# Performance work log

Measured on AMD Instinct MI355X. Metric: run time of the kernel, lower is better.

The kernel has to match this reference:

```python
import jax, jax.numpy as jnp
import numpy as np

B, C, H, W = 16, 64, 48, 48
D = C * W  # xLSTM embedding dim (== C*H since H==W)
K = 5          # phi='S' kernel size
G_CONV = C // 8  # conv groups = 8
G_NORM = 16      # GroupNorm groups
EPS = 1e-5


def setup_inputs() -> dict:
    key = jax.random.key(0)
    ks = jax.random.split(key, 10)
    s = 0.02
    return {
        'x': jax.random.normal(ks[0], (B, C, H, W), jnp.float32),
        'W1': (jax.random.normal(ks[1], (D, 4 * D), jnp.float32) * s),
        'R1': (jax.random.normal(ks[2], (D, 4 * D), jnp.float32) * s),
        'b1': jnp.zeros((4 * D,), jnp.float32),
        'W2': (jax.random.normal(ks[3], (D, 4 * D), jnp.float32) * s),
        'R2': (jax.random.normal(ks[4], (D, 4 * D), jnp.float32) * s),
        'b2': jnp.zeros((4 * D,), jnp.float32),
        'conv_w': jax.random.normal(ks[5], (C, C // G_CONV, K), jnp.float32) * (1.0 / np.sqrt((C // G_CONV) * K)),
        'gn_gamma': jnp.ones((C,), jnp.float32),
        'gn_beta': jnp.zeros((C,), jnp.float32),
    }


def xlstm_stack(x, Wm, Rm, bm):
    """sLSTM-style xLSTM block (exp gating + stabilizer). x: [B,T,D] -> [B,T,D]."""
    Bsz, T, Dm = x.shape
    pre = jnp.einsum('btd,de->bte', x, Wm) + bm  # input projection for all steps

    def step(carry, p):
        h, c, n, m = carry
        g = p + h @ Rm                      # [B,4D]
        it, ft, zt, ot = jnp.split(g, 4, axis=-1)
        m_new = jnp.maximum(ft + m, it)     # stabilizer
        i = jnp.exp(it - m_new)
        f = jnp.exp(ft + m - m_new)
        c_new = f * c + i * jnp.tanh(zt)
        n_new = f * n + i
        h_new = jax.nn.sigmoid(ot) * c_new / (n_new + 1e-6)
        return (h_new, c_new, n_new, m_new), h_new

    z = jnp.zeros((Bsz, Dm), x.dtype)
    _, ys = jax.lax.scan(step, (z, z, z, z), jnp.swapaxes(pre, 0, 1))
    return jnp.swapaxes(ys, 0, 1)  # [B,T,D]


def conv1d_grouped(x, w):
    pad = K // 2
    return jax.lax.conv_general_dilated(
        x, w, window_strides=(1,), padding=[(pad, pad)],
        feature_group_count=G_CONV, dimension_numbers=('NCH', 'OIH', 'NCH'))


def group_norm(x, gamma, beta):
    b, c, L = x.shape
    xg = x.reshape(b, G_NORM, -1)
    mu = xg.mean(-1, keepdims=True)
    var = xg.var(-1, keepdims=True)
    xn = ((xg - mu) * jax.lax.rsqrt(var + EPS)).reshape(b, c, L)
    return xn * gamma[None, :, None] + beta[None, :, None]


def ela_forward(x, W1, R1, b1, W2, R2, b2, conv_w, gn_gamma, gn_beta):
    b, c, h, w = x.shape
    # stack cfg2: sequence over h, features c*w
    y2 = xlstm_stack(x.reshape(b, h, c * w), W2, R2, b2).reshape(b, c, w, h)
    # stack cfg1: sequence over w, features c*h
    y1 = xlstm_stack(x.reshape(b, w, c * h), W1, R1, b1).reshape(b, c, w, h)
    x_h = jnp.mean(y2, axis=3).reshape(b, c, h)
    x_w = jnp.mean(y1, axis=2).reshape(b, c, w)
    x_h = jax.nn.sigmoid(group_norm(conv1d_grouped(x_h, conv_w), gn_gamma, gn_beta)).reshape(b, c, h, 1)
    x_w = jax.nn.sigmoid(group_norm(conv1d_grouped(x_w, conv_w), gn_gamma, gn_beta)).reshape(b, c, 1, w)
    return x_h * x_w * x


def reference(x, W1, R1, b1, W2, R2, b2, conv_w, gn_gamma, gn_beta):
    return ela_forward(x, W1, R1, b1, W2, R2, b2, conv_w, gn_gamma, gn_beta)
```

## Files before the change

### kernel.cpp

```cpp
#include <hip/hip_runtime.h>
#include <hip/hip_bf16.h>


typedef float  f32x4 __attribute__((ext_vector_type(4)));
typedef __bf16 v8bf  __attribute__((ext_vector_type(8)));
typedef __bf16 v4bf  __attribute__((ext_vector_type(4)));

#define MFMA16(a, b, c) __builtin_amdgcn_mfma_f32_16x16x32_bf16((a), (b), (c), 0, 0, 0)

static constexpr size_t OFF_PREP = 0;
static constexpr size_t SZ_PREP  = 37748736;
static constexpr size_t OFF_H0   = 37748736;
static constexpr size_t OFF_H1   = 37945344;
static constexpr size_t OFF_C    = 38141952;
static constexpr size_t OFF_N    = 38535168;
static constexpr size_t OFF_M    = 38928384;
static constexpr size_t OFF_YS   = 39321600;
static constexpr size_t OFF_GATE = 39714816;
static constexpr size_t BASE_END = 40108032;
static constexpr size_t SZ_RPACK = 75497472;
static constexpr size_t OFF_RA   = BASE_END;
static constexpr size_t OFF_RB   = BASE_END + SZ_RPACK;
static constexpr size_t END_A    = OFF_RB + SZ_RPACK;

__device__ __forceinline__ void gl_lds16(const void* g, void* l) {
    __builtin_amdgcn_global_load_lds(
        (const __attribute__((address_space(1))) unsigned int*)g,
        (__attribute__((address_space(3))) unsigned int*)l, 16, 0, 0);
}

__global__ __launch_bounds__(256) void zero_kernel(f32x4* __restrict__ p, int n) {
    int i = blockIdx.x * 256 + threadIdx.x;
    if (i < n) { f32x4 z = 0.0f; p[i] = z; }
}

__global__ __launch_bounds__(256) void pack_x_kernel(const float* __restrict__ x,
                                                     __bf16* __restrict__ dst) {
    int gi = blockIdx.x * 256 + threadIdx.x;
    int lane = gi & 63;
    int rest = gi >> 6;
    int sub = rest & 7; rest >>= 3;
    int kc = rest % 96, mb = rest / 96;
    int r = mb * 128 + sub * 16 + (lane & 15);
    int t = r >> 4, b = r & 15;
    int k = kc * 32 + (lane >> 4) * 8;
    const f32x4* s = (const f32x4*)(x + (size_t)b * 147456 + (size_t)t * 3072 + k);
    f32x4 v0 = s[0], v1 = s[1];
    v8bf o;
#pragma unroll
    for (int j = 0; j < 4; ++j) { o[j] = (__bf16)v0[j]; o[4 + j] = (__bf16)v1[j]; }
    ((v8bf*)dst)[gi] = o;
}

__global__ __launch_bounds__(256) void pack_B_kernel(const float* __restrict__ src0,
                                                     const float* __restrict__ src1,
                                                     __bf16* __restrict__ dst0,
                                                     __bf16* __restrict__ dst1) {
    int nb = blockIdx.x, kc = blockIdx.y, m = blockIdx.z;
    const float* src = m ? src1 : src0;
    __bf16* dst = m ? dst1 : dst0;
    int tid = threadIdx.x;
    __shared__ float tile[32][133];
    int kr = tid >> 3, nc0 = (tid & 7) * 16;
    const f32x4* s4 = (const f32x4*)(src + (size_t)(kc * 32 + kr) * 12288 + nb * 128 + nc0);
    f32x4 v0 = s4[0], v1 = s4[1], v2 = s4[2], v3 = s4[3];
#pragma unroll
    for (int r = 0; r < 4; ++r) {
        tile[kr][nc0 + r]      = v0[r];
        tile[kr][nc0 + 4 + r]  = v1[r];
        tile[kr][nc0 + 8 + r]  = v2[r];
        tile[kr][nc0 + 12 + r] = v3[r];
    }
    __syncthreads();
    __bf16* db = dst + (size_t)(nb * 96 + kc) * 4096;
#pragma unroll
    for (int c = 0; c < 2; ++c) {
        int lidx = tid * 2 + c;
        int sub = lidx >> 6, lane = lidx & 63;
        int kb = (lane >> 4) * 8, nn = sub * 16 + (lane & 15);
        v8bf o;
#pragma unroll
        for (int j = 0; j < 8; ++j) o[j] = (__bf16)tile[kb + j][nn];
        ((v8bf*)db)[lidx] = o;
    }
}

__global__ __launch_bounds__(256) void pre_gemm_packed(const __bf16* __restrict__ Apack,
                                                       const __bf16* __restrict__ Bp0,
                                                       const __bf16* __restrict__ Bp1,
                                                       __bf16* __restrict__ preP) {
    int nb = blockIdx.x, mb = blockIdx.y, stack = blockIdx.z;
    const char* Bpack = (const char*)(stack ? Bp1 : Bp0);
    int tid = threadIdx.x, wave = tid >> 6, lane = tid & 63;
    __shared__ alignas(16) __bf16 As[4096];
    __shared__ alignas(16) __bf16 Bs[4096];
    f32x4 acc[4][4];
#pragma unroll
    for (int i = 0; i < 4; ++i)
#pragma unroll
        for (int j = 0; j < 4; ++j) acc[i][j] = 0.0f;

    for (int kc = 0; kc < 96; ++kc) {
        size_t atile = (size_t)(mb * 96 + kc) * 8192;
        size_t btile = (size_t)(nb * 96 + kc) * 8192;
        int chunk = wave * 2048;
        gl_lds16((const char*)Apack + atile + chunk + lane * 16,        (char*)As + chunk);
        gl_lds16((const char*)Apack + atile + chunk + 1024 + lane * 16, (char*)As + chunk + 1024);
        gl_lds16(Bpack + btile + chunk + lane * 16,        (char*)Bs + chunk);
        gl_lds16(Bpack + btile + chunk + 1024 + lane * 16, (char*)Bs + chunk + 1024);
        __syncthreads();
        const v8bf* A8 = (const v8bf*)As;
        const v8bf* B8 = (const v8bf*)Bs;
        v8bf a[4], b[4];
#pragma unroll
        for (int mi = 0; mi < 4; ++mi) a[mi] = A8[((wave >> 1) * 4 + mi) * 64 + lane];
#pragma unroll
        for (int ni = 0; ni < 4; ++ni) b[ni] = B8[((wave & 1) * 4 + ni) * 64 + lane];
#pragma unroll
        for (int mi = 0; mi < 4; ++mi)
#pragma unroll
            for (int ni = 0; ni < 4; ++ni) acc[mi][ni] = MFMA16(a[mi], b[ni], acc[mi][ni]);
        __syncthreads();
    }
#pragma unroll
    for (int mi = 0; mi < 4; ++mi)
#pragma unroll
        for (int ni = 0; ni < 4; ++ni) {
            int mt = mb * 8 + (wave >> 1) * 4 + mi;
            int nt4 = nb * 8 + (wave & 1) * 4 + ni;
            v4bf o;
#pragma unroll
            for (int r = 0; r < 4; ++r) o[r] = (__bf16)acc[mi][ni][r];
            ((v4bf*)preP)[(((size_t)stack * 48 + mt) * 768 + nt4) * 64 + lane] = o;
        }
}

__global__ __launch_bounds__(256) void pre_gemm(const __bf16* __restrict__ Apack,
                                                const float* __restrict__ W1,
                                                const float* __restrict__ W2,
                                                __bf16* __restrict__ preP) {
    int nb = blockIdx.x, mb = blockIdx.y, stack = blockIdx.z;
    const float* W = stack ? W2 : W1;
    int tid = threadIdx.x, wave = tid >> 6, lane = tid & 63;
    __shared__ alignas(16) __bf16 As[4096];
    __shared__ alignas(16) __bf16 Bs[4096];
    __shared__ float tile[32][133];
    f32x4 acc[4][4];
#pragma unroll
    for (int i = 0; i < 4; ++i)
#pragma unroll
        for (int j = 0; j < 4; ++j) acc[i][j] = 0.0f;

    int kr = tid >> 3, nc0 = (tid & 7) * 16;
    for (int kc = 0; kc < 96; ++kc) {
        size_t atile = (size_t)(mb * 96 + kc) * 8192;
        int chunk = wave * 2048;
        gl_lds16((const char*)Apack + atile + chunk + lane * 16,        (char*)As + chunk);
        gl_lds16((const char*)Apack + atile + chunk + 1024 + lane * 16, (char*)As + chunk + 1024);
        const f32x4* s4 = (const f32x4*)(W + (size_t)(kc * 32 + kr) * 12288 + nb * 128 + nc0);
        f32x4 v0 = s4[0], v1 = s4[1], v2 = s4[2], v3 = s4[3];
#pragma unroll
        for (int r = 0; r < 4; ++r) {
            tile[kr][nc0 + r]      = v0[r];
            tile[kr][nc0 + 4 + r]  = v1[r];
            tile[kr][nc0 + 8 + r]  = v2[r];
            tile[kr][nc0 + 12 + r] = v3[r];
        }
        __syncthreads();
#pragma unroll
        for (int c = 0; c < 2; ++c) {
            int lidx = tid * 2 + c;
            int sub = lidx >> 6, l2 = lidx & 63;
            int kb = (l2 >> 4) * 8, nn = sub * 16 + (l2 & 15);
            v8bf o;
#pragma unroll
            for (int j = 0; j < 8; ++j) o[j] = (__bf16)tile[kb + j][nn];
            ((v8bf*)Bs)[lidx] = o;
        }
        __syncthreads();
        const v8bf* A8 = (const v8bf*)As;
        const v8bf* B8 = (const v8bf*)Bs;
        v8bf a[4], b[4];
#pragma unroll
        for (int mi = 0; mi < 4; ++mi) a[mi] = A8[((wave >> 1) * 4 + mi) * 64 + lane];
#pragma unroll
        for (int ni = 0; ni < 4; ++ni) b[ni] = B8[((wave & 1) * 4 + ni) * 64 + lane];
#pragma unroll
        for (int mi = 0; mi < 4; ++mi)
#pragma unroll
            for (int ni = 0; ni < 4; ++ni) acc[mi][ni] = MFMA16(a[mi], b[ni], acc[mi][ni]);
        __syncthreads();
    }
#pragma unroll
    for (int mi = 0; mi < 4; ++mi)
#pragma unroll
        for (int ni = 0; ni < 4; ++ni) {
            int mt = mb * 8 + (wave >> 1) * 4 + mi;
            int nt4 = nb * 8 + (wave & 1) * 4 + ni;
            v4bf o;
#pragma unroll
            for (int r = 0; r < 4; ++r) o[r] = (__bf16)acc[mi][ni][r];
            ((v4bf*)preP)[(((size_t)stack * 48 + mt) * 768 + nt4) * 64 + lane] = o;
        }
}

__global__ __launch_bounds__(512) void step_kernel(
    const __bf16* __restrict__ Rp0, const __bf16* __restrict__ Rp1,
    const __bf16* __restrict__ hread, __bf16* __restrict__ hwrite,
    const __bf16* __restrict__ preP,
    const float* __restrict__ bias1, const float* __restrict__ bias2,
    float* __restrict__ cbuf, float* __restrict__ nbuf, float* __restrict__ mbuf,
    float* __restrict__ ysum, int t) {
    int nt = blockIdx.x, stack = blockIdx.y;
    int tid = threadIdx.x, wave = tid >> 6, lane = tid & 63;
    const v8bf* Rp = (const v8bf*)(stack ? Rp1 : Rp0);
    const v8bf* hA = (const v8bf*)hread + (size_t)stack * 96 * 64;
    int sub = nt & 7;
    size_t base[4];
#pragma unroll
    for (int i = 0; i < 4; ++i) {
        int nb = i * 24 + (nt >> 3);
        base[i] = (size_t)nb * 49152 + (size_t)sub * 64 + lane;
    }
    int kcs = wave * 12;
    f32x4 acc[4];
#pragma unroll
    for (int i = 0; i < 4; ++i) acc[i] = 0.0f;

    v8bf aS[3];
    v8bf bS[3][4];
#pragma unroll
    for (int p = 0; p < 3; ++p) {
        int kc = kcs + p;
        aS[p] = hA[(size_t)kc * 64 + lane];
#pragma unroll
        for (int i = 0; i < 4; ++i) bS[p][i] = Rp[base[i] + (size_t)kc * 512];
    }
#pragma unroll
    for (int kk = 0; kk < 12; ++kk) {
        int sl = kk % 3;
#pragma unroll
        for (int i = 0; i < 4; ++i) acc[i] = MFMA16(aS[sl], bS[sl][i], acc[i]);
        if (kk < 9) {
            int kc = kcs + kk + 3;
            aS[sl] = hA[(size_t)kc * 64 + lane];
#pragma unroll
            for (int i = 0; i < 4; ++i) bS[sl][i] = Rp[base[i] + (size_t)kc * 512];
        }
    }

    __shared__ f32x4 red4[8][4][64];
#pragma unroll
    for (int i = 0; i < 4; ++i) red4[wave][i][lane] = acc[i];
    __syncthreads();

    if (wave == 0) {
        const float* bias = stack ? bias2 : bias1;
        f32x4 g[4];
#pragma unroll
        for (int i = 0; i < 4; ++i) {
            f32x4 s = red4[0][i][lane];
#pragma unroll
            for (int w = 1; w < 8; ++w) s += red4[w][i][lane];
            g[i] = s;
        }
        int fcol = nt * 16 + (lane & 15);
        int bq = (lane >> 4) * 4;
#pragma unroll
        for (int i = 0; i < 4; ++i) {
            v4bf pv = ((const v4bf*)preP)[(((size_t)stack * 48 + t) * 768 + (i * 192 + nt)) * 64 + lane];
            float bv = bias[i * 3072 + fcol];
#pragma unroll
            for (int r = 0; r < 4; ++r) g[i][r] += (float)pv[r] + bv;
        }
        size_t sidx = ((size_t)stack * 192 + nt) * 64 + lane;
        f32x4 cc = ((f32x4*)cbuf)[sidx];
        f32x4 nn = ((f32x4*)nbuf)[sidx];
        f32x4 mm = ((f32x4*)mbuf)[sidx];
        int kc = fcol >> 5, ko = fcol & 31;
        __bf16* hw = hwrite + ((size_t)stack * 96 + kc) * 512 + (size_t)(ko >> 3) * 128 + (ko & 7);
        int flat = t * 3072 + fcol;
        int cch = flat / 2304;
        int rem = flat - cch * 2304;
        int u = rem / 48;
        int v = rem - u * 48;
        int yidx = cch * 48 + (stack ? u : v);
        float* yb = ysum + (size_t)stack * 16 * 3072;
#pragma unroll
        for (int r = 0; r < 4; ++r) {
            int brow = bq + r;
            float it = g[0][r], ft = g[1][r], zt = g[2][r], ot = g[3][r];
            float mnew = fmaxf(ft + mm[r], it);
            float iv = __expf(it - mnew);
            float fv = __expf(ft + mm[r] - mnew);
            float cnew = fv * cc[r] + iv * tanhf(zt);
            float nnew = fv * nn[r] + iv;
            float sg = 1.0f / (1.0f + __expf(-ot));
            float h = sg * cnew / (nnew + 1e-6f);
            cc[r] = cnew; nn[r] = nnew; mm[r] = mnew;
            hw[(size_t)brow * 8] = (__bf16)h;
            atomicAdd(yb + (size_t)brow * 3072 + yidx, h);
        }
        ((f32x4*)cbuf)[sidx] = cc;
        ((f32x4*)nbuf)[sidx] = nn;
        ((f32x4*)mbuf)[sidx] = mm;
    }
}

__global__ __launch_bounds__(256) void conv_gn_kernel(const float* __restrict__ ysum,
                                                      const float* __restrict__ cw,
                                                      const float* __restrict__ gamma,
                                                      const float* __restrict__ beta,
                                                      float* __restrict__ gatebuf) {
    int bi = blockIdx.x;
    int s = bi >> 4, b = bi & 15;
    int tid = threadIdx.x;
    __shared__ float in0[3072], cvout[3072], cws[2560];
    __shared__ float r1[16][16], r2[16][16], mu_s[16], rs_s[16];
    const float* src = ysum + (size_t)(s * 16 + b) * 3072;
    for (int e = tid; e < 3072; e += 256) in0[e] = src[e] * (1.0f / 48.0f);
    for (int e = tid; e < 2560; e += 256) cws[e] = cw[e];
    __syncthreads();
    for (int e = tid; e < 3072; e += 256) {
        int co = e / 48, p = e - co * 48;
        int g = co >> 3;
        const float* wrow = cws + co * 40;
        const float* irow = in0 + g * 8 * 48;
        float a = 0.f;
#pragma unroll
        for (int ci = 0; ci < 8; ++ci)
#pragma unroll
            for (int q = 0; q < 5; ++q) {
                int pp = p + q - 2;
                if (pp >= 0 && pp < 48) a += wrow[ci * 5 + q] * irow[ci * 48 + pp];
            }
        cvout[e] = a;
    }
    __syncthreads();
    int gn = tid >> 4, ln = tid & 15;
    float s1 = 0.f, s2 = 0.f;
    for (int ii = ln; ii < 192; ii += 16) {
        float v = cvout[gn * 192 + ii];
        s1 += v; s2 += v * v;
    }
    r1[gn][ln] = s1; r2[gn][ln] = s2;
    __syncthreads();
    if (tid < 16) {
        float a = 0.f, c2 = 0.f;
        for (int ii = 0; ii < 16; ++ii) { a += r1[tid][ii]; c2 += r2[tid][ii]; }
        float mu = a * (1.0f / 192.0f);
        float var = c2 * (1.0f / 192.0f) - mu * mu;
        mu_s[tid] = mu;
        rs_s[tid] = rsqrtf(var + 1e-5f);
    }
    __syncthreads();
    float* dst = gatebuf + (size_t)(s * 16 + b) * 3072;
    for (int e = tid; e < 3072; e += 256) {
        int c = e / 48;
        int gg = c >> 2;
        float xn = (cvout[e] - mu_s[gg]) * rs_s[gg] * gamma[c] + beta[c];
        dst[e] = 1.0f / (1.0f + __expf(-xn));
    }
}

__global__ __launch_bounds__(256) void final_kernel(const float* __restrict__ x,
                                                    const float* __restrict__ gatebuf,
                                                    float* __restrict__ out) {
    int gid = blockIdx.x * 256 + threadIdx.x;
    int wi4 = gid % 12;
    int rest = gid / 12;
    int hi = rest % 48;
    int bc = rest / 48;
    int b = bc >> 6, c = bc & 63;
    f32x4 xv = ((const f32x4*)x)[gid];
    float gh = gatebuf[(size_t)(16 + b) * 3072 + c * 48 + hi];
    f32x4 gw = *(const f32x4*)(gatebuf + (size_t)b * 3072 + c * 48 + wi4 * 4);
    f32x4 o;
#pragma unroll
    for (int k = 0; k < 4; ++k) o[k] = xv[k] * gh * gw[k];
    ((f32x4*)out)[gid] = o;
}

extern "C" void kernel_launch(void* const* d_in, const int* in_sizes, int n_in,
                              void* d_out, int out_size, void* d_ws, size_t ws_size,
                              hipStream_t stream) {
    const float* x     = (const float*)d_in[0];
    const float* W1    = (const float*)d_in[1];
    const float* R1    = (const float*)d_in[2];
    const float* b1    = (const float*)d_in[3];
    const float* W2    = (const float*)d_in[4];
    const float* R2    = (const float*)d_in[5];
    const float* b2    = (const float*)d_in[6];
    const float* cw    = (const float*)d_in[7];
    const float* gamma = (const float*)d_in[8];
    const float* beta  = (const float*)d_in[9];

    char* ws = (char*)d_ws;
    __bf16* seqA = (__bf16*)d_out;
    __bf16* preP = (__bf16*)(ws + OFF_PREP);
    __bf16* h0   = (__bf16*)(ws + OFF_H0);
    __bf16* h1   = (__bf16*)(ws + OFF_H1);
    float* cbuf  = (float*)(ws + OFF_C);
    float* nbuf  = (float*)(ws + OFF_N);
    float* mbuf  = (float*)(ws + OFF_M);
    float* ysum  = (float*)(ws + OFF_YS);
    float* gate  = (float*)(ws + OFF_GATE);

    bool big_ws = ws_size >= END_A;
    __bf16* PA = (__bf16*)(ws + OFF_RA);
    __bf16* PB = (__bf16*)(ws + OFF_RB);

    pack_x_kernel<<<1152, 256, 0, stream>>>(x, seqA);
    if (big_ws) {
        pack_B_kernel<<<dim3(96, 96, 2), 256, 0, stream>>>(W1, W2, PA, PB);
        pre_gemm_packed<<<dim3(96, 6, 2), 256, 0, stream>>>(seqA, PA, PB, preP);
        pack_B_kernel<<<dim3(96, 96, 2), 256, 0, stream>>>(R1, R2, PA, PB);
    } else {
        pre_gemm<<<dim3(96, 6, 2), 256, 0, stream>>>(seqA, W1, W2, preP);
        pack_B_kernel<<<dim3(96, 96, 2), 256, 0, stream>>>(R1, R2, PA, PB);
    }
    zero_kernel<<<480, 256, 0, stream>>>((f32x4*)(ws + OFF_H0), 122880);
    for (int t = 0; t < 48; ++t) {
        const __bf16* hr = (t & 1) ? h1 : h0;
        __bf16* hw       = (t & 1) ? h0 : h1;
        step_kernel<<<dim3(192, 2), 512, 0, stream>>>(PA, PB, hr, hw, preP, b1, b2,
                                                      cbuf, nbuf, mbuf, ysum, t);
    }
    conv_gn_kernel<<<32, 256, 0, stream>>>(ysum, cw, gamma, beta, gate);
    final_kernel<<<2304, 256, 0, stream>>>(x, gate, (float*)d_out);
}
```

Measured before the change: 2.718 ms.

## Replace per-timestep launches with persistent cooperative kernel using grid sync

After: 9.199 ms. 238% more time.

```diff
diff --git a/kernel.cpp b/kernel.cpp
--- a/kernel.cpp
+++ b/kernel.cpp
@@ -1,5 +1,8 @@
 #include <hip/hip_runtime.h>
 #include <hip/hip_bf16.h>
+#include <hip/hip_cooperative_groups.h>
+
+namespace cg = cooperative_groups;
 
 
 typedef float  f32x4 __attribute__((ext_vector_type(4)));
@@ -135,73 +138,114 @@
         }
 }
 
-__global__ __launch_bounds__(256) void pre_gemm(const __bf16* __restrict__ Apack,
-                                                const float* __restrict__ W1,
-                                                const float* __restrict__ W2,
-                                                __bf16* __restrict__ preP) {
-    int nb = blockIdx.x, mb = blockIdx.y, stack = blockIdx.z;
-    const float* W = stack ? W2 : W1;
+__global__ __launch_bounds__(512) void persistent_step(
+    const __bf16* __restrict__ Rp0, const __bf16* __restrict__ Rp1,
+    __bf16* __restrict__ h0, __bf16* __restrict__ h1,
+    const __bf16* __restrict__ preP,
+    const float* __restrict__ bias1, const float* __restrict__ bias2,
+    float* __restrict__ ysum, f32x4* __restrict__ Gbuf) {
+    cg::grid_group grid = cg::this_grid();
+    int b = blockIdx.x;
     int tid = threadIdx.x, wave = tid >> 6, lane = tid & 63;
-    __shared__ alignas(16) __bf16 As[4096];
-    __shared__ alignas(16) __bf16 Bs[4096];
-    __shared__ float tile[32][133];
-    f32x4 acc[4][4];
-#pragma unroll
-    for (int i = 0; i < 4; ++i)
-#pragma unroll
-        for (int j = 0; j < 4; ++j) acc[i][j] = 0.0f;
-
-    int kr = tid >> 3, nc0 = (tid & 7) * 16;
-    for (int kc = 0; kc < 96; ++kc) {
-        size_t atile = (size_t)(mb * 96 + kc) * 8192;
-        int chunk = wave * 2048;
-        gl_lds16((const char*)Apack + atile + chunk + lane * 16,        (char*)As + chunk);
-        gl_lds16((const char*)Apack + atile + chunk + 1024 + lane * 16, (char*)As + chunk + 1024);
-        const f32x4* s4 = (const f32x4*)(W + (size_t)(kc * 32 + kr) * 12288 + nb * 128 + nc0);
-        f32x4 v0 = s4[0], v1 = s4[1], v2 = s4[2], v3 = s4[3];
-#pragma unroll
-        for (int r = 0; r < 4; ++r) {
-            tile[kr][nc0 + r]      = v0[r];
-            tile[kr][nc0 + 4 + r]  = v1[r];
-            tile[kr][nc0 + 8 + r]  = v2[r];
-            tile[kr][nc0 + 12 + r] = v3[r];
-        }
+
+    int stackA = b >> 7;
+    const v8bf* Rp = (const v8bf*)(stackA ? Rp1 : Rp0);
+    int ct0 = (b & 127) * 6;
+    size_t baseB[6];
+#pragma unroll
+    for (int i = 0; i < 6; ++i) {
+        int ct = ct0 + i;
+        baseB[i] = (size_t)(ct >> 3) * 49152 + (size_t)(ct & 7) * 64 + lane;
+    }
+    int kcs = wave * 12;
+
+    int u = -1;
+    if (wave == 0) u = b;
+    else if (wave == 1 && b < 128) u = 256 + b;
+    int su = 0, ntu = 0, fcol = 0, bq = 0, yidx = 0;
+    const float* biasB = bias1;
+    if (u >= 0) {
+        su = (u >= 192) ? 1 : 0;
+        ntu = u - su * 192;
+        fcol = ntu * 16 + (lane & 15);
+        bq = (lane >> 4) * 4;
+        biasB = su ? bias2 : bias1;
+    }
+    f32x4 cc = 0.0f, nn = 0.0f, mm = 0.0f;
+
+    const __bf16* hr = h0;
+    __bf16* hwp = h1;
+
+    __shared__ f32x4 red[8][6][64];
+
+    for (int t = 0; t < 48; ++t) {
+        const v8bf* hA = (const v8bf*)hr + (size_t)stackA * 96 * 64;
+        f32x4 acc[6];
+#pragma unroll
+        for (int i = 0; i < 6; ++i) acc[i] = 0.0f;
+#pragma unroll 4
+        for (int kk = 0; kk < 12; ++kk) {
+            int kc = kcs + kk;
+            v8bf a = hA[(size_t)kc * 64 + lane];
+            v8bf bb[6];
+#pragma unroll
+            for (int i = 0; i < 6; ++i) bb[i] = Rp[baseB[i] + (size_t)kc * 512];
+#pragma unroll
+            for (int i = 0; i < 6; ++i) acc[i] = MFMA16(a, bb[i], acc[i]);
+        }
+#pragma unroll
+        for (int i = 0; i < 6; ++i) red[wave][i][lane] = acc[i];
         __syncthreads();
-#pragma unroll
-        for (int c = 0; c < 2; ++c) {
-            int lidx = tid * 2 + c;
-            int sub = lidx >> 6, l2 = lidx & 63;
-            int kb = (l2 >> 4) * 8, nn = sub * 16 + (l2 & 15);
-            v8bf o;
-#pragma unroll
-            for (int j = 0; j < 8; ++j) o[j] = (__bf16)tile[kb + j][nn];
-            ((v8bf*)Bs)[lidx] = o;
-        }
-        __syncthreads();
-        const v8bf* A8 = (const v8bf*)As;
-        const v8bf* B8 = (const v8bf*)Bs;
-        v8bf a[4], b[4];
-#pragma unroll
-        for (int mi = 0; mi < 4; ++mi) a[mi] = A8[((wave >> 1) * 4 + mi) * 64 + lane];
-#pragma unroll
-        for (int ni = 0; ni < 4; ++ni) b[ni] = B8[((wave & 1) * 4 + ni) * 64 + lane];
-#pragma unroll
-        for (int mi = 0; mi < 4; ++mi)
-#pragma unroll
-            for (int ni = 0; ni < 4; ++ni) acc[mi][ni] = MFMA16(a[mi], b[ni], acc[mi][ni]);
-        __syncthreads();
-    }
-#pragma unroll
-    for (int mi = 0; mi < 4; ++mi)
-#pragma unroll
-        for (int ni = 0; ni < 4; ++ni) {
-            int mt = mb * 8 + (wave >> 1) * 4 + mi;
-            int nt4 = nb * 8 + (wave & 1) * 4 + ni;
-            v4bf o;
-#pragma unroll
-            for (int r = 0; r < 4; ++r) o[r] = (__bf16)acc[mi][ni][r];
-            ((v4bf*)preP)[(((size_t)stack * 48 + mt) * 768 + nt4) * 64 + lane] = o;
-        }
+        if (wave < 6) {
+            f32x4 s = red[0][wave][lane];
+#pragma unroll
+            for (int w = 1; w < 8; ++w) s += red[w][wave][lane];
+            Gbuf[(size_t)(b * 6 + wave) * 64 + lane] = s;
+        }
+        __threadfence();
+        grid.sync();
+
+        if (u >= 0) {
+            f32x4 g[4];
+#pragma unroll
+            for (int gi = 0; gi < 4; ++gi) {
+                int fid = su * 768 + gi * 192 + ntu;
+                g[gi] = Gbuf[(size_t)fid * 64 + lane];
+                v4bf pv = ((const v4bf*)preP)[(((size_t)su * 48 + t) * 768 + (gi * 192 + ntu)) * 64 + lane];
+                float bv = biasB[gi * 3072 + fcol];
+#pragma unroll
+                for (int r = 0; r < 4; ++r) g[gi][r] += (float)pv[r] + bv;
+            }
+            int kc2 = fcol >> 5, ko = fcol & 31;
+            __bf16* hwB = hwp + ((size_t)su * 96 + kc2) * 512 + (size_t)(ko >> 3) * 128 + (ko & 7);
+            int flat = t * 3072 + fcol;
+            int cch = flat / 2304;
+            int rem = flat - cch * 2304;
+            int uu = rem / 48;
+            int vv = rem - uu * 48;
+            yidx = cch * 48 + (su ? uu : vv);
+            float* yb = ysum + (size_t)su * 16 * 3072;
+#pragma unroll
+            for (int r = 0; r < 4; ++r) {
+                int brow = bq + r;
+                float it = g[0][r], ft = g[1][r], zt = g[2][r], ot = g[3][r];
+                float mnew = fmaxf(ft + mm[r], it);
+                float iv = __expf(it - mnew);
+                float fv = __expf(ft + mm[r] - mnew);
+                float cnew = fv * cc[r] + iv * tanhf(zt);
+                float nnew = fv * nn[r] + iv;
+                float sg = 1.0f / (1.0f + __expf(-ot));
+                float h = sg * cnew / (nnew + 1e-6f);
+                cc[r] = cnew; nn[r] = nnew; mm[r] = mnew;
+                hwB[(size_t)brow * 8] = (__bf16)h;
+                atomicAdd(yb + (size_t)brow * 3072 + yidx, h);
+            }
+        }
+        __threadfence();
+        grid.sync();
+
+        const __bf16* tmp = hr; hr = hwp; hwp = (__bf16*)tmp;
+    }
 }
 
 __global__ __launch_bounds__(512) void step_kernel(
@@ -226,27 +270,15 @@
     f32x4 acc[4];
 #pragma unroll
     for (int i = 0; i < 4; ++i) acc[i] = 0.0f;
-
-    v8bf aS[3];
-    v8bf bS[3][4];
-#pragma unroll
-    for (int p = 0; p < 3; ++p) {
-        int kc = kcs + p;
-        aS[p] = hA[(size_t)kc * 64 + lane];
-#pragma unroll
-        for (int i = 0; i < 4; ++i) bS[p][i] = Rp[base[i] + (size_t)kc * 512];
-    }
-#pragma unroll
+#pragma unroll 4
     for (int kk = 0; kk < 12; ++kk) {
-        int sl = kk % 3;
-#pragma unroll
-        for (int i = 0; i < 4; ++i) acc[i] = MFMA16(aS[sl], bS[sl][i], acc[i]);
-        if (kk < 9) {
-            int kc = kcs + kk + 3;
-            aS[sl] = hA[(size_t)kc * 64 + lane];
-#pragma unroll
-            for (int i = 0; i < 4; ++i) bS[sl][i] = Rp[base[i] + (size_t)kc * 512];
-        }
+        int kc = kcs + kk;
+        v8bf a = hA[(size_t)kc * 64 + lane];
+        v8bf bb[4];
+#pragma unroll
+        for (int i = 0; i < 4; ++i) bb[i] = Rp[base[i] + (size_t)kc * 512];
+#pragma unroll
+        for (int i = 0; i < 4; ++i) acc[i] = MFMA16(a, bb[i], acc[i]);
     }
 
     __shared__ f32x4 red4[8][4][64];
@@ -282,9 +314,9 @@
         int flat = t * 3072 + fcol;
         int cch = flat / 2304;
         int rem = flat - cch * 2304;
-        int u = rem / 48;
-        int v = rem - u * 48;
-        int yidx = cch * 48 + (stack ? u : v);
+        int uu = rem / 48;
+        int vv = rem - uu * 48;
+        int yidx = cch * 48 + (stack ? uu : vv);
         float* yb = ysum + (size_t)stack * 16 * 3072;
 #pragma unroll
         for (int r = 0; r < 4; ++r) {
@@ -405,6 +437,7 @@
     float* mbuf  = (float*)(ws + OFF_M);
     float* ysum  = (float*)(ws + OFF_YS);
     float* gate  = (float*)(ws + OFF_GATE);
+    f32x4* gbuf  = (f32x4*)d_out;
 
     bool big_ws = ws_size >= END_A;
     __bf16* PA = (__bf16*)(ws + OFF_RA);
@@ -416,16 +449,32 @@
         pre_gemm_packed<<<dim3(96, 6, 2), 256, 0, stream>>>(seqA, PA, PB, preP);
         pack_B_kernel<<<dim3(96, 96, 2), 256, 0, stream>>>(R1, R2, PA, PB);
     } else {
-        pre_gemm<<<dim3(96, 6, 2), 256, 0, stream>>>(seqA, W1, W2, preP);
         pack_B_kernel<<<dim3(96, 96, 2), 256, 0, stream>>>(R1, R2, PA, PB);
+        pre_gemm_packed<<<dim3(96, 6, 2), 256, 0, stream>>>(seqA, PA, PB, preP);
     }
     zero_kernel<<<480, 256, 0, stream>>>((f32x4*)(ws + OFF_H0), 122880);
-    for (int t = 0; t < 48; ++t) {
-        const __bf16* hr = (t & 1) ? h1 : h0;
-        __bf16* hw       = (t & 1) ? h0 : h1;
-        step_kernel<<<dim3(192, 2), 512, 0, stream>>>(PA, PB, hr, hw, preP, b1, b2,
-                                                      cbuf, nbuf, mbuf, ysum, t);
-    }
+
+    {
+        const __bf16* a0 = PA; const __bf16* a1 = PB;
+        __bf16* ph0 = h0; __bf16* ph1 = h1;
+        const __bf16* pp = preP;
+        const float* pb1 = b1; const float* pb2 = b2;
+        float* pys = ysum; f32x4* pg = gbuf;
+        void* args[] = { (void*)&a0, (void*)&a1, (void*)&ph0, (void*)&ph1,
+                         (void*)&pp, (void*)&pb1, (void*)&pb2, (void*)&pys, (void*)&pg };
+        hipError_t err = hipLaunchCooperativeKernel(
+            reinterpret_cast<void*>(persistent_step), dim3(256), dim3(512),
+            args, 0, stream);
+        if (err != hipSuccess) {
+            for (int t = 0; t < 48; ++t) {
+                const __bf16* hr = (t & 1) ? h1 : h0;
+                __bf16* hw       = (t & 1) ? h0 : h1;
+                step_kernel<<<dim3(192, 2), 512, 0, stream>>>(PA, PB, hr, hw, preP, b1, b2,
+                                                              cbuf, nbuf, mbuf, ysum, t);
+            }
+        }
+    }
+
     conv_gn_kernel<<<32, 256, 0, stream>>>(ysum, cw, gamma, beta, gate);
     final_kernel<<<2304, 256, 0, stream>>>(x, gate, (float*)d_out);
 }
```
